# Performance work log

Hardware: AMD Instinct MI355X
Metric: run time of the kernel (lower is better)

## Reference

```python
import jax, jax.numpy as jnp
import numpy as np

N = 100000      # nodes (single ntype)
F_IN = 128
F_OUT = 128
R = 3           # relations
E = 262144      # edges per relation
LRELU_SLOPE = 0.2


def setup_inputs() -> dict:
    key = jax.random.key(0)
    ks = jax.random.split(key, 6)
    x = jax.random.normal(ks[0], (N, F_IN), jnp.float32)
    src = jax.random.randint(ks[1], (R, E), 0, N)
    dst = jax.random.randint(ks[2], (R, E), 0, N)
    # attention: Linear(2*in_feat, 1) per relation
    att_w = jax.random.normal(ks[3], (R, 2 * F_IN, 1), jnp.float32) * 0.05
    att_b = jnp.zeros((R, 1), jnp.float32)
    # transform: Linear(in_feat, out_feat) per relation
    tw = jax.random.normal(ks[4], (R, F_IN, F_OUT), jnp.float32) * (1.0 / np.sqrt(F_IN))
    tb = jnp.zeros((R, F_OUT), jnp.float32)
    h_bias = jnp.zeros((F_OUT,), jnp.float32)
    return dict(x=x, att_w=att_w, att_b=att_b, tw=tw, tb=tb,
                h_bias=h_bias, src=src, dst=dst)


def reference(x, att_w, att_b, tw, tb, h_bias, src, dst):
    # Per-relation gather of endpoint features.  [R, E, F_IN]
    h_src = x[src]
    h_dst = x[dst]
    # attention Linear on cat([h_src, h_dst]) == split matmul (avoids concat)
    w_s, w_d = att_w[:, :F_IN, :], att_w[:, F_IN:, :]
    scores = (jnp.einsum('ref,rfo->reo', h_src, w_s)
              + jnp.einsum('ref,rfo->reo', h_dst, w_d)
              + att_b[:, None, :])                      # [R, E, 1]
    scores = jax.nn.leaky_relu(scores, negative_slope=LRELU_SLOPE)
    # Faithful to source: F.softmax(scores, dim=0) -> softmax over ALL edges
    # of a relation (NOT per-destination edge softmax).
    a = jax.nn.softmax(scores, axis=1)                  # [R, E, 1]
    # u_mul_e with node-level transform(h_src): message = (h_src @ tw + tb) * a
    msg = (jnp.einsum('ref,rfo->reo', h_src, tw) + tb[:, None, :]) * a  # [R,E,F_OUT]
    # scatter-sum to destinations per relation, then sum over relations
    agg = jax.vmap(lambda m, d: jax.ops.segment_sum(m, d, num_segments=N))(msg, dst)
    h = agg.sum(axis=0) + h_bias                        # [N, F_OUT]
    # activation=relu, dropout=0.0 (identity)
    return jax.nn.relu(h)
```

## Files before the change

### kernel.cpp

```cpp
#include <hip/hip_runtime.h>
#include <hip/hip_bf16.h>

#define N_NODES 100000
#define FDIM 128
#define RREL 3
#define NEDGE 262144
#define SLOPE 0.2f
#define NCHUNK 98
#define PROJ_BLOCKS (N_NODES / 8)
#define HIST_BLOCKS (RREL * NEDGE / 256)

typedef __attribute__((ext_vector_type(8))) short bf16x8;
typedef __attribute__((ext_vector_type(8))) unsigned short u16x8;
typedef __attribute__((ext_vector_type(4))) float f32x4;
typedef __attribute__((ext_vector_type(4))) int i32x4;

__device__ inline unsigned short f2bf(float f) {
    __hip_bfloat16 h = __float2bfloat16(f);
    return *reinterpret_cast<unsigned short*>(&h);
}
__device__ inline float bf2f(unsigned short u) {
    unsigned int b = ((unsigned int)u) << 16;
    return __int_as_float(b);
}

#define WS_PS    0
#define WS_PD    300000
#define WS_SUMS  600000
#define WS_COUNT 600016
#define WS_ROWS  900016
#define WS_BSUM  1200016
#define WS_ESORT 1200528
#define WS_ASUM  2773392
#define WS_TWT   3073392
#define WS_TBS   3097968
#define WS_XBF   3098352
#define WS_AGGB  9498352
#define WS_RANK  28698352

__global__ void proj_hist_kernel(const float* __restrict__ x,
                                 const float* __restrict__ att_w,
                                 float* __restrict__ ps, float* __restrict__ pd,
                                 unsigned short* __restrict__ x_bf,
                                 const int* __restrict__ dst, int* __restrict__ count,
                                 int* __restrict__ rank) {
    if (blockIdx.x >= PROJ_BLOCKS) {
        const int b = blockIdx.x - PROJ_BLOCKS;
        const int gid = b * 256 + threadIdx.x;
        const int r = b >> 10;
        rank[gid] = atomicAdd(&count[r * N_NODES + dst[gid]], 1);
        return;
    }
    const int lane = threadIdx.x & 31;
    const int n = blockIdx.x * 8 + (threadIdx.x >> 5);
    const float4 xv = *reinterpret_cast<const float4*>(x + (size_t)n * FDIM + lane * 4);
    ushort4 u;
    u.x = f2bf(xv.x); u.y = f2bf(xv.y); u.z = f2bf(xv.z); u.w = f2bf(xv.w);
    *reinterpret_cast<ushort4*>(x_bf + (size_t)n * FDIM + lane * 4) = u;
    float accs[RREL], accd[RREL];
#pragma unroll
    for (int r = 0; r < RREL; ++r) {
        const float4 wsv = *reinterpret_cast<const float4*>(att_w + r * 2 * FDIM + lane * 4);
        const float4 wdv = *reinterpret_cast<const float4*>(att_w + r * 2 * FDIM + FDIM + lane * 4);
        accs[r] = xv.x * wsv.x + xv.y * wsv.y + xv.z * wsv.z + xv.w * wsv.w;
        accd[r] = xv.x * wdv.x + xv.y * wdv.y + xv.z * wdv.z + xv.w * wdv.w;
    }
#pragma unroll
    for (int off = 16; off >= 1; off >>= 1) {
#pragma unroll
        for (int r = 0; r < RREL; ++r) {
            accs[r] += __shfl_xor(accs[r], off);
            accd[r] += __shfl_xor(accd[r], off);
        }
    }
    if (lane == 0) {
#pragma unroll
        for (int r = 0; r < RREL; ++r) {
            ps[r * N_NODES + n] = accs[r];
            pd[r * N_NODES + n] = accd[r];
        }
    }
}

__global__ void scan1_kernel(const int* __restrict__ count, int* __restrict__ row_start,
                             int* __restrict__ bsum) {
    const int r = blockIdx.x / NCHUNK;
    const int b = blockIdx.x % NCHUNK;
    const int tid = threadIdx.x;
    const int base = b * 1024 + tid * 4;
    int v[4];
#pragma unroll
    for (int i = 0; i < 4; ++i)
        v[i] = (base + i < N_NODES) ? count[r * N_NODES + base + i] : 0;
    const int tsum = v[0] + v[1] + v[2] + v[3];
    __shared__ int sd[256];
    sd[tid] = tsum;
    __syncthreads();
    for (int off = 1; off < 256; off <<= 1) {
        const int tv = (tid >= off) ? sd[tid - off] : 0;
        __syncthreads();
        sd[tid] += tv;
        __syncthreads();
    }
    int run = sd[tid] - tsum;
#pragma unroll
    for (int i = 0; i < 4; ++i) {
        if (base + i < N_NODES) row_start[r * N_NODES + base + i] = run;
        run += v[i];
    }
    if (tid == 255) bsum[blockIdx.x] = sd[255];
}

__global__ void scan2_kernel(int* __restrict__ bsum) {
    const int r = blockIdx.x;
    const int tid = threadIdx.x;
    const int v = (tid < NCHUNK) ? bsum[r * NCHUNK + tid] : 0;
    __shared__ int sd[256];
    sd[tid] = v;
    __syncthreads();
    for (int off = 1; off < 256; off <<= 1) {
        const int tv = (tid >= off) ? sd[tid - off] : 0;
        __syncthreads();
        sd[tid] += tv;
        __syncthreads();
    }
    if (tid < NCHUNK) bsum[r * NCHUNK + tid] = sd[tid] - v;
}

__global__ void scan3_kernel(int* __restrict__ row_start, const int* __restrict__ bsum) {
    const int r = blockIdx.x / NCHUNK;
    const int b = blockIdx.x % NCHUNK;
    const int add = bsum[blockIdx.x];
    const int base = b * 1024 + threadIdx.x * 4;
#pragma unroll
    for (int i = 0; i < 4; ++i)
        if (base + i < N_NODES) row_start[r * N_NODES + base + i] += add;
}

__global__ void fill_kernel(const int* __restrict__ src, const int* __restrict__ dst,
                            const float* __restrict__ ps, const float* __restrict__ pd,
                            const float* __restrict__ att_b,
                            const int* __restrict__ row_start, const int* __restrict__ rank,
                            int2* __restrict__ edge_sorted, float* __restrict__ sums) {
    const int gid = blockIdx.x * 256 + threadIdx.x;
    const int r = blockIdx.x >> 10;
    const int s = src[gid];
    const int d = dst[gid];
    float sc = ps[r * N_NODES + s] + pd[r * N_NODES + d] + att_b[r];
    sc = sc > 0.f ? sc : SLOPE * sc;
    const float ev = __expf(sc);
    const int pos = row_start[r * N_NODES + d] + rank[gid];
    int2 pk;
    pk.x = s;
    pk.y = __float_as_int(ev);
    edge_sorted[(size_t)r * NEDGE + pos] = pk;
    float v = ev;
#pragma unroll
    for (int off = 32; off >= 1; off >>= 1) v += __shfl_xor(v, off);
    __shared__ float red[4];
    if ((threadIdx.x & 63) == 0) red[threadIdx.x >> 6] = v;
    __syncthreads();
    if (threadIdx.x == 0) {
        unsafeAtomicAdd(&sums[r], red[0] + red[1] + red[2] + red[3]);
    }
}

__global__ void cast_kernel(const float* __restrict__ tw, const float* __restrict__ tb,
                            const float* __restrict__ sums,
                            unsigned short* __restrict__ twT, float* __restrict__ tbs) {
    const int c = blockIdx.x;
    const int kk = threadIdx.x;
    const float inv = 1.0f / sums[kk >> 7];
    twT[c * 384 + kk] = f2bf(tw[kk * 128 + c] * inv);
    if (c == 0) tbs[kk] = tb[kk] * inv;
}

__global__ void agg_kernel(const int* __restrict__ row_start,
                           const int2* __restrict__ edge_sorted,
                           const unsigned short* __restrict__ x_bf,
                           unsigned short* __restrict__ aggb, float* __restrict__ asum) {
    const int lane = threadIdx.x & 15;
    const int r = blockIdx.y;
    const int n = blockIdx.x * 16 + (threadIdx.x >> 4);
    const int beg = row_start[r * N_NODES + n];
    const int end = (n == N_NODES - 1) ? NEDGE : row_start[r * N_NODES + n + 1];
    const int2* es = edge_sorted + (size_t)r * NEDGE;

    float acc[8] = {0.f, 0.f, 0.f, 0.f, 0.f, 0.f, 0.f, 0.f};
    float asacc = 0.f;

    for (int i = beg; i < end; i += 4) {
        const int rem = end - i;
        int2 pk0, pk1, pk2, pk3;
        pk0 = es[i];
        if (rem > 1) pk1 = es[i + 1];
        if (rem > 2) pk2 = es[i + 2];
        if (rem > 3) pk3 = es[i + 3];
        u16x8 xv0, xv1, xv2, xv3;
        xv0 = *reinterpret_cast<const u16x8*>(x_bf + (size_t)pk0.x * FDIM + lane * 8);
        if (rem > 1) xv1 = *reinterpret_cast<const u16x8*>(x_bf + (size_t)pk1.x * FDIM + lane * 8);
        if (rem > 2) xv2 = *reinterpret_cast<const u16x8*>(x_bf + (size_t)pk2.x * FDIM + lane * 8);
        if (rem > 3) xv3 = *reinterpret_cast<const u16x8*>(x_bf + (size_t)pk3.x * FDIM + lane * 8);
        {
            const float a = __int_as_float(pk0.y);
            asacc += a;
#pragma unroll
            for (int d = 0; d < 8; ++d) acc[d] += a * bf2f(xv0[d]);
        }
        if (rem > 1) {
            const float a = __int_as_float(pk1.y);
            asacc += a;
#pragma unroll
            for (int d = 0; d < 8; ++d) acc[d] += a * bf2f(xv1[d]);
        }
        if (rem > 2) {
            const float a = __int_as_float(pk2.y);
            asacc += a;
#pragma unroll
            for (int d = 0; d < 8; ++d) acc[d] += a * bf2f(xv2[d]);
        }
        if (rem > 3) {
            const float a = __int_as_float(pk3.y);
            asacc += a;
#pragma unroll
            for (int d = 0; d < 8; ++d) acc[d] += a * bf2f(xv3[d]);
        }
    }

    u16x8 o;
#pragma unroll
    for (int d = 0; d < 8; ++d) o[d] = f2bf(acc[d]);
    i32x4* dst4 = reinterpret_cast<i32x4*>(aggb + (size_t)n * 384 + r * FDIM + lane * 8);
    __builtin_nontemporal_store(*reinterpret_cast<i32x4*>(&o), dst4);
    if (lane == 0) asum[r * N_NODES + n] = asacc;
}

__global__ __launch_bounds__(256, 4)
void gemm_kernel(const unsigned short* __restrict__ A, const unsigned short* __restrict__ Bt,
                 const float* __restrict__ asum, const float* __restrict__ tbs,
                 const float* __restrict__ h_bias, float* __restrict__ out) {
    __shared__ unsigned short sA[2][128 * 40];
    __shared__ unsigned short sB[2][128 * 40];
    const int tid = threadIdx.x;
    const int row0 = blockIdx.x * 128;
    const int rs = tid >> 2;
    const int koff = (tid & 3) * 8;

#pragma unroll
    for (int i = 0; i < 2; ++i) {
        const int rc = rs + i * 64;
        const int grow = row0 + rc;
        int4 va = {0, 0, 0, 0};
        if (grow < N_NODES)
            va = *reinterpret_cast<const int4*>(&A[(size_t)grow * 384 + koff]);
        *reinterpret_cast<int4*>(&sA[0][rc * 40 + koff]) = va;
        const int4 vb = *reinterpret_cast<const int4*>(&Bt[rc * 384 + koff]);
        *reinterpret_cast<int4*>(&sB[0][rc * 40 + koff]) = vb;
    }
    __syncthreads();

    const int w = tid >> 6, l = tid & 63;
    const int lr = l & 15, lk = l >> 4;
    f32x4 acc[2][8];
#pragma unroll
    for (int rt = 0; rt < 2; ++rt)
#pragma unroll
        for (int ct = 0; ct < 8; ++ct) acc[rt][ct] = (f32x4){0.f, 0.f, 0.f, 0.f};

    for (int ks = 0; ks < 12; ++ks) {
        const int buf = ks & 1;
        int4 ra[2], rb[2];
        if (ks < 11) {
            const int k0 = (ks + 1) * 32;
#pragma unroll
            for (int i = 0; i < 2; ++i) {
                const int rc = rs + i * 64;
                const int grow = row0 + rc;
                ra[i] = make_int4(0, 0, 0, 0);
                if (grow < N_NODES)
                    ra[i] = *reinterpret_cast<const int4*>(&A[(size_t)grow * 384 + k0 + koff]);
                rb[i] = *reinterpret_cast<const int4*>(&Bt[rc * 384 + k0 + koff]);
            }
        }
        bf16x8 afr[2];
#pragma unroll
        for (int rt = 0; rt < 2; ++rt)
            afr[rt] = *reinterpret_cast<const bf16x8*>(&sA[buf][(w * 32 + rt * 16 + lr) * 40 + lk * 8]);
#pragma unroll
        for (int ct = 0; ct < 8; ++ct) {
            const bf16x8 bfr = *reinterpret_cast<const bf16x8*>(&sB[buf][(ct * 16 + lr) * 40 + lk * 8]);
            acc[0][ct] = __builtin_amdgcn_mfma_f32_16x16x32_bf16(afr[0], bfr, acc[0][ct], 0, 0, 0);
            acc[1][ct] = __builtin_amdgcn_mfma_f32_16x16x32_bf16(afr[1], bfr, acc[1][ct], 0, 0, 0);
        }
        if (ks < 11) {
#pragma unroll
            for (int i = 0; i < 2; ++i) {
                const int rc = rs + i * 64;
                *reinterpret_cast<int4*>(&sA[buf ^ 1][rc * 40 + koff]) = ra[i];
                *reinterpret_cast<int4*>(&sB[buf ^ 1][rc * 40 + koff]) = rb[i];
            }
        }
        __syncthreads();
    }

#pragma unroll
    for (int rt = 0; rt < 2; ++rt) {
        const int rowbase = row0 + w * 32 + rt * 16 + lk * 4;
        float as[RREL][4];
#pragma unroll
        for (int r = 0; r < RREL; ++r)
#pragma unroll
            for (int j = 0; j < 4; ++j)
                as[r][j] = (rowbase + j < N_NODES) ? asum[r * N_NODES + rowbase + j] : 0.f;
#pragma unroll
        for (int ct = 0; ct < 8; ++ct) {
            const int col = ct * 16 + lr;
            const float hb = h_bias[col];
            const float t0 = tbs[col], t1 = tbs[FDIM + col], t2 = tbs[2 * FDIM + col];
#pragma unroll
            for (int j = 0; j < 4; ++j) {
                const int row = rowbase + j;
                if (row < N_NODES) {
                    float v = acc[rt][ct][j] + as[0][j] * t0 + as[1][j] * t1 + as[2][j] * t2 + hb;
                    out[(size_t)row * FDIM + col] = fmaxf(v, 0.f);
                }
            }
        }
    }
}

extern "C" void kernel_launch(void* const* d_in, const int* in_sizes, int n_in,
                              void* d_out, int out_size, void* d_ws, size_t ws_size,
                              hipStream_t stream) {
    const float* x      = (const float*)d_in[0];
    const float* att_w  = (const float*)d_in[1];
    const float* att_b  = (const float*)d_in[2];
    const float* tw     = (const float*)d_in[3];
    const float* tb     = (const float*)d_in[4];
    const float* h_bias = (const float*)d_in[5];
    const int*   src    = (const int*)d_in[6];
    const int*   dst    = (const int*)d_in[7];
    float* out = (float*)d_out;

    float* wsf = (float*)d_ws;
    float* ps         = wsf + WS_PS;
    float* pd         = wsf + WS_PD;
    float* sums       = wsf + WS_SUMS;
    int*   count      = (int*)(wsf + WS_COUNT);
    int*   row_start  = (int*)(wsf + WS_ROWS);
    int*   bsum       = (int*)(wsf + WS_BSUM);
    int2*  edge_sorted= (int2*)(wsf + WS_ESORT);
    float* asum       = wsf + WS_ASUM;
    unsigned short* twT  = (unsigned short*)(wsf + WS_TWT);
    float* tbs        = wsf + WS_TBS;
    unsigned short* x_bf = (unsigned short*)(wsf + WS_XBF);
    unsigned short* aggb = (unsigned short*)(wsf + WS_AGGB);
    int*   rank       = (int*)(wsf + WS_RANK);

    hipMemsetAsync(sums, 0, 16 * sizeof(float), stream);
    hipMemsetAsync(count, 0, (size_t)RREL * N_NODES * sizeof(int), stream);

    proj_hist_kernel<<<PROJ_BLOCKS + HIST_BLOCKS, 256, 0, stream>>>(x, att_w, ps, pd, x_bf,
                                                                    dst, count, rank);

    scan1_kernel<<<RREL * NCHUNK, 256, 0, stream>>>(count, row_start, bsum);
    scan2_kernel<<<RREL, 256, 0, stream>>>(bsum);
    scan3_kernel<<<RREL * NCHUNK, 256, 0, stream>>>(row_start, bsum);

    fill_kernel<<<RREL * NEDGE / 256, 256, 0, stream>>>(src, dst, ps, pd, att_b,
                                                        row_start, rank, edge_sorted, sums);

    cast_kernel<<<FDIM, 384, 0, stream>>>(tw, tb, sums, twT, tbs);

    agg_kernel<<<dim3(N_NODES / 16, RREL), 256, 0, stream>>>(row_start, edge_sorted, x_bf,
                                                             aggb, asum);

    gemm_kernel<<<(N_NODES + 127) / 128, 256, 0, stream>>>(aggb, twT, asum, tbs, h_bias, out);
}
```

Baseline: 211.6 us.

## Compute attention projections with bf16 MFMA over 128-row LDS tiles

The per-node attention dot products, previously a warp-shuffle reduction per node, now run as a small GEMM on MFMA. Each block stages 128 bf16 rows of x and a padded 16x128 bf16 weight tile in LDS and computes all six projections at once. The block count drops from one block per 8 nodes to 782 blocks of 128 rows, and launch bounds are added. The aim is to cut shuffle and reduction overhead, but the projections are now computed from bf16-rounded x and weights, which changes precision slightly.

After: 194.6 us. -8.0%, faster.

```diff
diff --git a/kernel.cpp b/kernel.cpp
--- a/kernel.cpp
+++ b/kernel.cpp
@@ -7,7 +7,7 @@
 #define NEDGE 262144
 #define SLOPE 0.2f
 #define NCHUNK 98
-#define PROJ_BLOCKS (N_NODES / 8)
+#define PROJ_BLOCKS 782
 #define HIST_BLOCKS (RREL * NEDGE / 256)
 
 typedef __attribute__((ext_vector_type(8))) short bf16x8;
@@ -38,12 +38,13 @@
 #define WS_AGGB  9498352
 #define WS_RANK  28698352
 
-__global__ void proj_hist_kernel(const float* __restrict__ x,
-                                 const float* __restrict__ att_w,
-                                 float* __restrict__ ps, float* __restrict__ pd,
-                                 unsigned short* __restrict__ x_bf,
-                                 const int* __restrict__ dst, int* __restrict__ count,
-                                 int* __restrict__ rank) {
+__global__ __launch_bounds__(256, 4)
+void proj_hist_kernel(const float* __restrict__ x,
+                      const float* __restrict__ att_w,
+                      float* __restrict__ ps, float* __restrict__ pd,
+                      unsigned short* __restrict__ x_bf,
+                      const int* __restrict__ dst, int* __restrict__ count,
+                      int* __restrict__ rank) {
     if (blockIdx.x >= PROJ_BLOCKS) {
         const int b = blockIdx.x - PROJ_BLOCKS;
         const int gid = b * 256 + threadIdx.x;
@@ -51,33 +52,60 @@
         rank[gid] = atomicAdd(&count[r * N_NODES + dst[gid]], 1);
         return;
     }
-    const int lane = threadIdx.x & 31;
-    const int n = blockIdx.x * 8 + (threadIdx.x >> 5);
-    const float4 xv = *reinterpret_cast<const float4*>(x + (size_t)n * FDIM + lane * 4);
-    ushort4 u;
-    u.x = f2bf(xv.x); u.y = f2bf(xv.y); u.z = f2bf(xv.z); u.w = f2bf(xv.w);
-    *reinterpret_cast<ushort4*>(x_bf + (size_t)n * FDIM + lane * 4) = u;
-    float accs[RREL], accd[RREL];
-#pragma unroll
-    for (int r = 0; r < RREL; ++r) {
-        const float4 wsv = *reinterpret_cast<const float4*>(att_w + r * 2 * FDIM + lane * 4);
-        const float4 wdv = *reinterpret_cast<const float4*>(att_w + r * 2 * FDIM + FDIM + lane * 4);
-        accs[r] = xv.x * wsv.x + xv.y * wsv.y + xv.z * wsv.z + xv.w * wsv.w;
-        accd[r] = xv.x * wdv.x + xv.y * wdv.y + xv.z * wdv.z + xv.w * wdv.w;
-    }
-#pragma unroll
-    for (int off = 16; off >= 1; off >>= 1) {
-#pragma unroll
-        for (int r = 0; r < RREL; ++r) {
-            accs[r] += __shfl_xor(accs[r], off);
-            accd[r] += __shfl_xor(accd[r], off);
-        }
-    }
-    if (lane == 0) {
-#pragma unroll
-        for (int r = 0; r < RREL; ++r) {
-            ps[r * N_NODES + n] = accs[r];
-            pd[r * N_NODES + n] = accd[r];
+    __shared__ unsigned short sX[128 * 136];
+    __shared__ unsigned short sW[16 * 136];
+    const int tid = threadIdx.x;
+    const int row0 = blockIdx.x * 128;
+
+#pragma unroll
+    for (int i = 0; i < 8; ++i) {
+        const int idx = tid + i * 256;
+        const int c = idx >> 7, k = idx & 127;
+        float v = 0.f;
+        if (c < 3) v = att_w[c * 256 + k];
+        else if (c < 6) v = att_w[(c - 3) * 256 + 128 + k];
+        sW[c * 136 + k] = f2bf(v);
+    }
+    const int g = tid >> 5, lane = tid & 31;
+#pragma unroll
+    for (int it = 0; it < 16; ++it) {
+        const int rrow = it * 8 + g;
+        const int row = row0 + rrow;
+        float4 xv = make_float4(0.f, 0.f, 0.f, 0.f);
+        if (row < N_NODES) xv = *reinterpret_cast<const float4*>(x + (size_t)row * FDIM + lane * 4);
+        ushort4 u;
+        u.x = f2bf(xv.x); u.y = f2bf(xv.y); u.z = f2bf(xv.z); u.w = f2bf(xv.w);
+        if (row < N_NODES)
+            *reinterpret_cast<ushort4*>(x_bf + (size_t)row * FDIM + lane * 4) = u;
+        *reinterpret_cast<ushort4*>(&sX[rrow * 136 + lane * 4]) = u;
+    }
+    __syncthreads();
+
+    const int w = tid >> 6, l = tid & 63;
+    const int lr = l & 15, lk = l >> 4;
+    f32x4 acc[2];
+    acc[0] = (f32x4){0.f, 0.f, 0.f, 0.f};
+    acc[1] = (f32x4){0.f, 0.f, 0.f, 0.f};
+#pragma unroll
+    for (int ks = 0; ks < 4; ++ks) {
+        const bf16x8 bfr = *reinterpret_cast<const bf16x8*>(&sW[lr * 136 + ks * 32 + lk * 8]);
+#pragma unroll
+        for (int rt = 0; rt < 2; ++rt) {
+            const bf16x8 afr =
+                *reinterpret_cast<const bf16x8*>(&sX[(w * 32 + rt * 16 + lr) * 136 + ks * 32 + lk * 8]);
+            acc[rt] = __builtin_amdgcn_mfma_f32_16x16x32_bf16(afr, bfr, acc[rt], 0, 0, 0);
+        }
+    }
+    if (lr < 6) {
+        float* base = (lr < 3) ? (ps + lr * N_NODES) : (pd + (lr - 3) * N_NODES);
+#pragma unroll
+        for (int rt = 0; rt < 2; ++rt) {
+            const int rowbase = row0 + w * 32 + rt * 16 + lk * 4;
+#pragma unroll
+            for (int j = 0; j < 4; ++j) {
+                const int row = rowbase + j;
+                if (row < N_NODES) base[row] = acc[rt][j];
+            }
         }
     }
 }
```
